# Performance work log

Hardware: AMD Instinct MI355X
Metric: run time of the kernel (lower is better)

The kernel has to match this reference:

```python
import jax, jax.numpy as jnp
import numpy as np

N = 8192
D_IN = 256
D_OUT = 256
DROP_P = 0.5


def setup_inputs() -> dict:
    key = jax.random.key(0)
    k1, k2, k3, k4, k5 = jax.random.split(key, 5)
    inputs = jax.random.normal(k1, (N, D_IN), dtype=jnp.float32)
    # torch nn.Linear weights are [d_out, d_in], applied as x @ W.T
    Wq = jax.random.normal(k2, (D_OUT, D_IN), dtype=jnp.float32) * (1.0 / np.sqrt(D_IN))
    Wk = jax.random.normal(k3, (D_OUT, D_IN), dtype=jnp.float32) * (1.0 / np.sqrt(D_IN))
    Wv = jax.random.normal(k4, (D_OUT, D_IN), dtype=jnp.float32) * (1.0 / np.sqrt(D_IN))
    # deterministic dropout keep-mask (True = keep), p=0.5
    drop_mask = jax.random.bernoulli(k5, 1.0 - DROP_P, (N, N))
    return {"inputs": inputs, "Wq": Wq, "Wk": Wk, "Wv": Wv, "drop_mask": drop_mask}


def reference(inputs, Wq, Wk, Wv, drop_mask):
    # QKV projections (no bias)
    q = inputs @ Wq.T  # [N, d_out]
    k = inputs @ Wk.T  # [N, d_out]
    v = inputs @ Wv.T  # [N, d_out]

    d_k = k.shape[1]
    scores = q @ k.T  # [N, N]

    # causal mask: strictly-upper-triangular entries -> -inf
    n = scores.shape[0]
    causal = jnp.triu(jnp.ones((n, n), dtype=bool), k=1)
    masked = jnp.where(causal, -jnp.inf, scores)

    attn_weights = jax.nn.softmax(masked / jnp.sqrt(jnp.float32(d_k)), axis=-1)

    # dropout p=0.5 in train mode: zero dropped entries, scale kept by 1/(1-p)
    scale = jnp.float32(1.0 / (1.0 - DROP_P))
    attn_weights = jnp.where(drop_mask, attn_weights * scale, 0.0)

    context_vector = attn_weights @ v  # [N, d_out]
    return context_vector
```

## Files before the change

### kernel.cpp

```cpp
#include <hip/hip_runtime.h>

#define NT 8192
#define DM 256

typedef float f32x16 __attribute__((ext_vector_type(16)));
typedef float f32x4 __attribute__((ext_vector_type(4)));
typedef __bf16 bf16x8 __attribute__((ext_vector_type(8)));
typedef unsigned int u32x4 __attribute__((ext_vector_type(4)));

#define MFMA32(a, b, c) __builtin_amdgcn_mfma_f32_32x32x16_bf16((a), (b), (c), 0, 0, 0)
#define MFMA16(a, b, c) __builtin_amdgcn_mfma_f32_16x16x32_bf16((a), (b), (c), 0, 0, 0)
#define NEG_INF (-__builtin_inff())

static __device__ __forceinline__ unsigned short f2bf_bits(float f) {
  return __builtin_bit_cast(unsigned short, (__bf16)f);
}
static __device__ __forceinline__ float exp2_fast(float x) {
  return __builtin_amdgcn_exp2f(x);
}
static __device__ __forceinline__ void gload_lds16(const void* g, void* l) {
  __builtin_amdgcn_global_load_lds(
      (const __attribute__((address_space(1))) unsigned int*)g,
      (__attribute__((address_space(3))) unsigned int*)l, 16, 0, 0);
}

__global__ __launch_bounds__(256) void maskpack_kernel(
    const void* __restrict__ mask, unsigned long long* __restrict__ bm) {
  const int t = threadIdx.x, lane = t & 63, w = t >> 6;
  const int r = blockIdx.x + (w << 11);
  const unsigned int* md = (const unsigned int*)mask;
  bool a01 = true, af = true;
#pragma unroll
  for (int k = 0; k < 4; ++k) {
    unsigned int v = md[lane + 64 * k];
    a01 = a01 && (v <= 1u);
    af = af && (v == 0u || v == 0x3F800000u);
  }
  const bool dword_mode = __all(a01) || __all(af);
  unsigned long long* out = bm + (size_t)r * 128;
  if (dword_mode) {
    const unsigned int* mk = (const unsigned int*)mask + (size_t)r * NT;
    const int iters = (r >> 8) + 1;
    for (int it = 0; it < iters; ++it) {
      const int j0 = it * 256;
      unsigned int v0 = mk[j0 + lane];
      unsigned int v1 = mk[j0 + 64 + lane];
      unsigned int v2 = mk[j0 + 128 + lane];
      unsigned int v3 = mk[j0 + 192 + lane];
      unsigned long long b0 = __ballot(v0 != 0u);
      unsigned long long b1 = __ballot(v1 != 0u);
      unsigned long long b2 = __ballot(v2 != 0u);
      unsigned long long b3 = __ballot(v3 != 0u);
      if (lane == 0) {
        out[(j0 >> 6) + 0] = b0;
        out[(j0 >> 6) + 1] = b1;
        out[(j0 >> 6) + 2] = b2;
        out[(j0 >> 6) + 3] = b3;
      }
    }
  } else {
    const unsigned char* mk = (const unsigned char*)mask + (size_t)r * NT;
    unsigned short* outs = (unsigned short*)out;
    const int iters = (r >> 10) + 1;
    for (int it = 0; it < iters; ++it) {
      const uint4 d = *(const uint4*)(mk + it * 1024 + lane * 16);
      unsigned int dws[4] = {d.x, d.y, d.z, d.w};
      unsigned int m16 = 0;
#pragma unroll
      for (int k = 0; k < 4; ++k) {
        unsigned int x = dws[k];
        x |= x >> 4;
        x |= x >> 2;
        x |= x >> 1;
        x &= 0x01010101u;
        m16 |= ((x * 0x01020408u) >> 24) << (4 * k);
      }
      outs[it * 64 + lane] = (unsigned short)m16;
    }
  }
}

__global__ __launch_bounds__(256) void proj_kernel(
    const float* __restrict__ X, const float* __restrict__ Wq,
    const float* __restrict__ Wk, const float* __restrict__ Wv,
    unsigned short* __restrict__ Qs, unsigned short* __restrict__ Kb,
    unsigned short* __restrict__ Vt) {
  __shared__ __align__(16) unsigned short Xs[64 * 256];
  __shared__ __align__(16) unsigned short Ws[64 * 256];
  __shared__ float Tr[4][32 * 33];
  const int ib = blockIdx.x, mat = blockIdx.y;
  const float* W = (mat == 0) ? Wq : (mat == 1) ? Wk : Wv;
  const float wscale = (mat == 0) ? 0.09016844005556021f : (mat == 2 ? 2.0f : 1.0f);
  const int t = threadIdx.x;
  const int lane = t & 63, w = t >> 6;
  const int m = lane & 31, half = lane >> 5;
  const int i0 = ib * 64;
#pragma unroll
  for (int cc = 0; cc < 8; ++cc) {
    int chunk = t + 256 * cc;
    int rr = chunk >> 5, c = chunk & 31;
    const float4* src = (const float4*)(X + (size_t)(i0 + rr) * 256 + c * 8);
    float4 f0 = src[0], f1 = src[1];
    bf16x8 v;
    v[0] = (__bf16)f0.x; v[1] = (__bf16)f0.y; v[2] = (__bf16)f0.z; v[3] = (__bf16)f0.w;
    v[4] = (__bf16)f1.x; v[5] = (__bf16)f1.y; v[6] = (__bf16)f1.z; v[7] = (__bf16)f1.w;
    *(bf16x8*)&Xs[(rr * 32 + (c ^ (rr & 31))) * 8] = v;
  }
  const int wr = w >> 1, wc = w & 1;
  for (int cb = 0; cb < 4; ++cb) {
    __syncthreads();
#pragma unroll
    for (int cc = 0; cc < 8; ++cc) {
      int chunk = t + 256 * cc;
      int rr = chunk >> 5, c = chunk & 31;
      const float4* src = (const float4*)(W + (size_t)(cb * 64 + rr) * 256 + c * 8);
      float4 f0 = src[0], f1 = src[1];
      bf16x8 v;
      v[0] = (__bf16)(f0.x * wscale); v[1] = (__bf16)(f0.y * wscale);
      v[2] = (__bf16)(f0.z * wscale); v[3] = (__bf16)(f0.w * wscale);
      v[4] = (__bf16)(f1.x * wscale); v[5] = (__bf16)(f1.y * wscale);
      v[6] = (__bf16)(f1.z * wscale); v[7] = (__bf16)(f1.w * wscale);
      *(bf16x8*)&Ws[(rr * 32 + (c ^ (rr & 31))) * 8] = v;
    }
    __syncthreads();
    f32x16 acc = {};
    const int ar = 32 * wr + m;
    const int br = 32 * wc + m;
#pragma unroll
    for (int st = 0; st < 16; ++st) {
      int kc = st * 2 + half;
      bf16x8 a = *(const bf16x8*)&Xs[(ar * 32 + (kc ^ (ar & 31))) * 8];
      bf16x8 b = *(const bf16x8*)&Ws[(br * 32 + (kc ^ (br & 31))) * 8];
      acc = MFMA32(a, b, acc);
    }
    if (mat < 2) {
      unsigned short* O = mat ? Kb : Qs;
#pragma unroll
      for (int r = 0; r < 16; ++r) {
        int row = i0 + 32 * wr + (r & 3) + 8 * (r >> 2) + 4 * half;
        int col = cb * 64 + 32 * wc + m;
        O[(size_t)row * DM + col] = f2bf_bits(acc[r]);
      }
    } else {
      float* T = Tr[w];
#pragma unroll
      for (int r = 0; r < 16; ++r) {
        int rl = (r & 3) + 8 * (r >> 2) + 4 * half;
        T[m * 33 + rl] = acc[r];
      }
      asm volatile("s_waitcnt lgkmcnt(0)" ::: "memory");
#pragma unroll
      for (int q = 0; q < 16; ++q) {
        int dl = 2 * q + half;
        float val = T[dl * 33 + m];
        Vt[(size_t)(cb * 64 + 32 * wc + dl) * NT + i0 + 32 * wr + m] = f2bf_bits(val);
      }
      asm volatile("s_waitcnt lgkmcnt(0)" ::: "memory");
    }
  }
}

__global__ __launch_bounds__(256, 3) void flash_kernel(
    const unsigned short* __restrict__ Qs, const unsigned short* __restrict__ Kg,
    const unsigned short* __restrict__ Vtg, const unsigned int* __restrict__ bm,
    float* __restrict__ ml_out, unsigned short* __restrict__ acc_out) {
  __shared__ __align__(16) unsigned short Ksh[32 * 256];
  __shared__ __align__(16) unsigned short Vsh[256 * 32];
  const int ib = blockIdx.x;
  const int seg = blockIdx.y;
  const int jb_end = 2 * (ib + 1);
  const int jb0 = seg * 16;
  if (jb0 >= jb_end) return;
  const int jb1 = (jb0 + 16 < jb_end) ? jb0 + 16 : jb_end;
  const int t = threadIdx.x, lane = t & 63, w = t >> 6;
  const int m = lane & 15, q = lane >> 4;
  const int i0 = ib * 64, rw0 = i0 + 16 * w;
  const int myrow = rw0 + m;

  bf16x8 qf[8];
  {
    const unsigned short* qp = Qs + (size_t)myrow * DM + q * 8;
#pragma unroll
    for (int st = 0; st < 8; ++st) qf[st] = *(const bf16x8*)(qp + st * 32);
  }
  f32x4 oacc[16] = {};
  float mrun = -1e30f, lrun = 0.f;

#define STAGE(JB)                                                             \
  {                                                                           \
    const int j32_ = (JB) * 32;                                               \
    _Pragma("unroll") for (int i_ = 0; i_ < 4; ++i_) {                        \
      int chunk = t + 256 * i_;                                               \
      int row = chunk >> 5, slot = chunk & 31;                                \
      gload_lds16(Kg + (size_t)(j32_ + row) * DM + (slot ^ row) * 8,          \
                  Ksh + (size_t)chunk * 8);                                   \
    }                                                                         \
    _Pragma("unroll") for (int i_ = 0; i_ < 4; ++i_) {                        \
      int chunk = t + 256 * i_;                                               \
      int d_ = chunk >> 2, slot = chunk & 3;                                  \
      gload_lds16(Vtg + (size_t)d_ * NT + j32_ + (slot ^ (d_ & 3)) * 8,       \
                  Vsh + (size_t)chunk * 8);                                   \
    }                                                                         \
  }

  STAGE(jb0)
  unsigned int bits = bm[(size_t)myrow * 256 + jb0];
  for (int jb = jb0; jb < jb1; ++jb) {
    const int j32 = jb * 32;
    __syncthreads();
    if (j32 <= rw0 + 15) {
      f32x4 s[2] = {};
#pragma unroll
      for (int st = 0; st < 8; ++st) {
        int kc = st * 4 + q;
#pragma unroll
        for (int ct = 0; ct < 2; ++ct) {
          int jr = ct * 16 + m;
          bf16x8 a = *(const bf16x8*)&Ksh[(jr * 32 + (kc ^ jr)) * 8];
          s[ct] = MFMA16(a, qf[st], s[ct]);
        }
      }
      if (j32 + 31 > rw0) {
#pragma unroll
        for (int ct = 0; ct < 2; ++ct)
#pragma unroll
          for (int r = 0; r < 4; ++r)
            if (j32 + ct * 16 + q * 4 + r > myrow) s[ct][r] = NEG_INF;
      }
      float mx = fmaxf(fmaxf(fmaxf(s[0][0], s[0][1]), fmaxf(s[0][2], s[0][3])),
                       fmaxf(fmaxf(s[1][0], s[1][1]), fmaxf(s[1][2], s[1][3])));
      mx = fmaxf(mx, __shfl_xor(mx, 16));
      mx = fmaxf(mx, __shfl_xor(mx, 32));
      const float mn = fmaxf(mrun, mx);
#pragma unroll
      for (int ct = 0; ct < 2; ++ct)
#pragma unroll
        for (int r = 0; r < 4; ++r) s[ct][r] = exp2_fast(s[ct][r] - mn);
      float rs = (s[0][0] + s[0][1]) + (s[0][2] + s[0][3]) +
                 (s[1][0] + s[1][1]) + (s[1][2] + s[1][3]);
      rs += __shfl_xor(rs, 16);
      rs += __shfl_xor(rs, 32);
      if (__all(mn == mrun)) {
        lrun += rs;
      } else {
        float alpha = exp2_fast(mrun - mn);
        lrun = lrun * alpha + rs;
#pragma unroll
        for (int ct = 0; ct < 16; ++ct)
#pragma unroll
          for (int r = 0; r < 4; ++r) oacc[ct][r] *= alpha;
        mrun = mn;
      }
      unsigned int A0, A1, B0, B1;
      {
        unsigned int bbA = bits >> (q * 4);
        unsigned int bbB = bits >> (16 + q * 4);
        float a0 = (bbA & 1u) ? s[0][0] : 0.f, a1 = (bbA & 2u) ? s[0][1] : 0.f;
        float a2 = (bbA & 4u) ? s[0][2] : 0.f, a3 = (bbA & 8u) ? s[0][3] : 0.f;
        float b0 = (bbB & 1u) ? s[1][0] : 0.f, b1 = (bbB & 2u) ? s[1][1] : 0.f;
        float b2 = (bbB & 4u) ? s[1][2] : 0.f, b3 = (bbB & 8u) ? s[1][3] : 0.f;
        A0 = (unsigned)f2bf_bits(a0) | ((unsigned)f2bf_bits(a1) << 16);
        A1 = (unsigned)f2bf_bits(a2) | ((unsigned)f2bf_bits(a3) << 16);
        B0 = (unsigned)f2bf_bits(b0) | ((unsigned)f2bf_bits(b1) << 16);
        B1 = (unsigned)f2bf_bits(b2) | ((unsigned)f2bf_bits(b3) << 16);
      }
      unsigned int own0 = (q & 2) ? B0 : A0, own1 = (q & 2) ? B1 : A1;
      unsigned int sA0 = (q & 2) ? A0 : B0, sA1 = (q & 2) ? A1 : B1;
      unsigned int r10 = __shfl_xor(sA0, 32);
      unsigned int r11 = __shfl_xor(sA1, 32);
      const bool selOwn = ((q ^ (q >> 1)) & 1) != 0;
      unsigned int s20 = selOwn ? own0 : r10;
      unsigned int s21 = selOwn ? own1 : r11;
      unsigned int r20 = __shfl_xor(s20, 16);
      unsigned int r21 = __shfl_xor(s21, 16);
      unsigned int lo0 = (q == 0) ? own0 : (q == 2) ? r10 : r20;
      unsigned int lo1 = (q == 0) ? own1 : (q == 2) ? r11 : r21;
      unsigned int hi0 = (q == 3) ? own0 : (q == 1) ? r10 : r20;
      unsigned int hi1 = (q == 3) ? own1 : (q == 1) ? r11 : r21;
      bf16x8 pf = __builtin_bit_cast(bf16x8, (u32x4){lo0, lo1, hi0, hi1});
#pragma unroll
      for (int ct = 0; ct < 16; ++ct) {
        int d = ct * 16 + m;
        bf16x8 a = *(const bf16x8*)&Vsh[(d * 4 + (q ^ (d & 3))) * 8];
        oacc[ct] = MFMA16(a, pf, oacc[ct]);
      }
    }
    __syncthreads();
    if (jb + 1 < jb1) {
      STAGE(jb + 1)
      bits = bm[(size_t)myrow * 256 + jb + 1];
    }
  }
#undef STAGE
  const int a_ = ib >> 3, r_ = ib & 7;
  const int g = 4 * a_ * (a_ + 1) + r_ * (a_ + 1) + seg;
  if (q == 0) {
    float* mlb = ml_out + ((size_t)g * 64 + 16 * w + m) * 2;
    mlb[0] = mrun;
    mlb[1] = lrun;
  }
  unsigned short* ab = acc_out + ((size_t)g * 64 + 16 * w + m) * DM;
#pragma unroll
  for (int ct = 0; ct < 16; ++ct) {
    unsigned long long pk = 0;
#pragma unroll
    for (int r = 0; r < 4; ++r)
      pk |= (unsigned long long)f2bf_bits(oacc[ct][r]) << (16 * r);
    *(unsigned long long*)&ab[ct * 16 + q * 4] = pk;
  }
}

__global__ __launch_bounds__(256) void combine_kernel(
    const float* __restrict__ ml, const unsigned short* __restrict__ pacc,
    float* __restrict__ out) {
  const int t = threadIdx.x;
  const int row = blockIdx.x * 32 + (t >> 3);
  const int cg = (t & 7) * 32;
  const int ib = row >> 6, rib = row & 63;
  const int a = ib >> 3, r = ib & 7;
  const int g0 = 4 * a * (a + 1) + r * (a + 1);
  const int ns = a + 1;
  float M = -1e30f;
  for (int s = 0; s < ns; ++s) M = fmaxf(M, ml[((size_t)(g0 + s) * 64 + rib) * 2]);
  float Wd = 0.f;
  float acc[32];
#pragma unroll
  for (int j = 0; j < 32; ++j) acc[j] = 0.f;
  for (int s = 0; s < ns; ++s) {
    const float* mls = ml + ((size_t)(g0 + s) * 64 + rib) * 2;
    float wv = exp2_fast(mls[0] - M);
    Wd += wv * mls[1];
    const unsigned short* pa = pacc + ((size_t)(g0 + s) * 64 + rib) * DM + cg;
#pragma unroll
    for (int v4 = 0; v4 < 4; ++v4) {
      bf16x8 b = *(const bf16x8*)(pa + v4 * 8);
#pragma unroll
      for (int j = 0; j < 8; ++j) acc[v4 * 8 + j] += wv * (float)b[j];
    }
  }
  float inv = 1.0f / Wd;
#pragma unroll
  for (int j = 0; j < 32; ++j) out[(size_t)row * DM + cg + j] = acc[j] * inv;
}

extern "C" void kernel_launch(void* const* d_in, const int* in_sizes, int n_in,
                              void* d_out, int out_size, void* d_ws, size_t ws_size,
                              hipStream_t stream) {
  const float* X  = (const float*)d_in[0];
  const float* Wq = (const float*)d_in[1];
  const float* Wk = (const float*)d_in[2];
  const float* Wv = (const float*)d_in[3];
  const void* mask = d_in[4];
  float* out = (float*)d_out;

  char* ws = (char*)d_ws;
  unsigned short* Qs = (unsigned short*)(ws + 4096);
  unsigned short* Kb = Qs + (size_t)NT * DM;
  unsigned short* Vt = Kb + (size_t)NT * DM;
  float* ml = (float*)(Vt + (size_t)NT * DM);
  unsigned short* pacc = (unsigned short*)(ml + (size_t)1088 * 64 * 2);
  unsigned long long* bmw = (unsigned long long*)((char*)pacc + (size_t)1088 * 64 * DM * 2);

  maskpack_kernel<<<2048, 256, 0, stream>>>(mask, bmw);
  proj_kernel<<<dim3(128, 3), 256, 0, stream>>>(X, Wq, Wk, Wv, Qs, Kb, Vt);
  flash_kernel<<<dim3(128, 16), 256, 0, stream>>>(Qs, Kb, Vt, (const unsigned int*)bmw,
                                                  ml, pacc);
  combine_kernel<<<256, 256, 0, stream>>>(ml, pacc, out);
}
```

Baseline: 467.1 us.

## Double-buffer K tiles and overlap V/K loads with QK and softmax compute

```diff
diff --git a/kernel.cpp b/kernel.cpp
--- a/kernel.cpp
+++ b/kernel.cpp
@@ -164,7 +164,7 @@
     const unsigned short* __restrict__ Qs, const unsigned short* __restrict__ Kg,
     const unsigned short* __restrict__ Vtg, const unsigned int* __restrict__ bm,
     float* __restrict__ ml_out, unsigned short* __restrict__ acc_out) {
-  __shared__ __align__(16) unsigned short Ksh[32 * 256];
+  __shared__ __align__(16) unsigned short Ksh[2][32 * 256];
   __shared__ __align__(16) unsigned short Vsh[256 * 32];
   const int ib = blockIdx.x;
   const int seg = blockIdx.y;
@@ -186,15 +186,19 @@
   f32x4 oacc[16] = {};
   float mrun = -1e30f, lrun = 0.f;
 
-#define STAGE(JB)                                                             \
+#define STAGE_K(JB, B)                                                        \
   {                                                                           \
     const int j32_ = (JB) * 32;                                               \
     _Pragma("unroll") for (int i_ = 0; i_ < 4; ++i_) {                        \
       int chunk = t + 256 * i_;                                               \
       int row = chunk >> 5, slot = chunk & 31;                                \
       gload_lds16(Kg + (size_t)(j32_ + row) * DM + (slot ^ row) * 8,          \
-                  Ksh + (size_t)chunk * 8);                                   \
+                  &Ksh[B][(size_t)chunk * 8]);                                \
     }                                                                         \
+  }
+#define STAGE_V(JB)                                                           \
+  {                                                                           \
+    const int j32_ = (JB) * 32;                                               \
     _Pragma("unroll") for (int i_ = 0; i_ < 4; ++i_) {                        \
       int chunk = t + 256 * i_;                                               \
       int d_ = chunk >> 2, slot = chunk & 3;                                  \
@@ -203,12 +207,24 @@
     }                                                                         \
   }
 
-  STAGE(jb0)
+  STAGE_K(jb0, 0)
   unsigned int bits = bm[(size_t)myrow * 256 + jb0];
   for (int jb = jb0; jb < jb1; ++jb) {
+    const int buf = (jb - jb0) & 1;
     const int j32 = jb * 32;
-    __syncthreads();
-    if (j32 <= rw0 + 15) {
+    const bool has_next = (jb + 1 < jb1);
+    asm volatile("s_waitcnt vmcnt(0)" ::: "memory");
+    __builtin_amdgcn_s_barrier();
+    STAGE_V(jb)
+    unsigned int bits_next = 0;
+    if (has_next) {
+      STAGE_K(jb + 1, buf ^ 1)
+      bits_next = bm[(size_t)myrow * 256 + jb + 1];
+    }
+    const bool live = (j32 <= rw0 + 15);
+    bf16x8 pf;
+    if (live) {
+      const unsigned short* Kb_ = Ksh[buf];
       f32x4 s[2] = {};
 #pragma unroll
       for (int st = 0; st < 8; ++st) {
@@ -216,7 +232,7 @@
 #pragma unroll
         for (int ct = 0; ct < 2; ++ct) {
           int jr = ct * 16 + m;
-          bf16x8 a = *(const bf16x8*)&Ksh[(jr * 32 + (kc ^ jr)) * 8];
+          bf16x8 a = *(const bf16x8*)&Kb_[(jr * 32 + (kc ^ jr)) * 8];
           s[ct] = MFMA16(a, qf[st], s[ct]);
         }
       }
@@ -277,7 +293,15 @@
       unsigned int lo1 = (q == 0) ? own1 : (q == 2) ? r11 : r21;
       unsigned int hi0 = (q == 3) ? own0 : (q == 1) ? r10 : r20;
       unsigned int hi1 = (q == 3) ? own1 : (q == 1) ? r11 : r21;
-      bf16x8 pf = __builtin_bit_cast(bf16x8, (u32x4){lo0, lo1, hi0, hi1});
+      pf = __builtin_bit_cast(bf16x8, (u32x4){lo0, lo1, hi0, hi1});
+    }
+    if (has_next) {
+      asm volatile("s_waitcnt vmcnt(5)" ::: "memory");
+    } else {
+      asm volatile("s_waitcnt vmcnt(0)" ::: "memory");
+    }
+    __builtin_amdgcn_s_barrier();
+    if (live) {
 #pragma unroll
       for (int ct = 0; ct < 16; ++ct) {
         int d = ct * 16 + m;
@@ -285,13 +309,10 @@
         oacc[ct] = MFMA16(a, pf, oacc[ct]);
       }
     }
-    __syncthreads();
-    if (jb + 1 < jb1) {
-      STAGE(jb + 1)
-      bits = bm[(size_t)myrow * 256 + jb + 1];
-    }
-  }
-#undef STAGE
+    bits = bits_next;
+  }
+#undef STAGE_K
+#undef STAGE_V
   const int a_ = ib >> 3, r_ = ib & 7;
   const int g = 4 * a_ * (a_ + 1) + r_ * (a_ + 1) + seg;
   if (q == 0) {
```

Measured after the change: 500.0 us. 1.07x slower.
